# Kernel tuning notes

Hardware: AMD Instinct MI355X
Metric: run time of the kernel (lower is better)

Reference implementation:

```python
import jax, jax.numpy as jnp
import numpy as np

N, P, F, R, M = 20000, 320000, 128, 64, 32
F4 = F // 4            # n_atombasis // 4 == graph_n_messagebasis
L1 = 2                 # max_multipole_order + 1 (charges + dipoles)
N_BLOCKS = 2


def _w(key, fan_in, fan_out):
    return jax.random.normal(key, (fan_in, fan_out), dtype=jnp.float32) / np.sqrt(fan_in)


def setup_inputs() -> dict:
    key = jax.random.key(0)
    ks = jax.random.split(key, 24)
    inp = {
        'features': jax.random.normal(ks[0], (N, F), dtype=jnp.float32),
        'distances': jax.random.uniform(ks[1], (P,), dtype=jnp.float32),
        'vectors': jax.random.normal(ks[2], (P, 3), dtype=jnp.float32),
        'cutoffs': jax.random.uniform(ks[3], (P,), dtype=jnp.float32),
        'rbfs': jax.random.normal(ks[4], (P, R), dtype=jnp.float32),
        'idx_i': jnp.sort(jax.random.randint(ks[5], (P,), 0, N)),
        'idx_j': jax.random.randint(ks[6], (P,), 0, N),
    }
    d_inv = 6 * F4 + 2 * F   # (n_features_anisotropic+1)*(F//4) + 2*F = 448
    d_eq0 = F4 + 2 * F       # 288
    inp['Wrbf'] = _w(ks[7], R + 2 * F, F4)
    inp['Wemb'] = _w(ks[8], F, F)
    inp['eq0_W1'] = _w(ks[9], d_eq0, F)
    inp['eq0_b1'] = jnp.zeros((F,), jnp.float32)
    inp['eq0_W2'] = _w(ks[10], F, M * L1) * 0.01
    inp['eq1_W1'] = _w(ks[11], d_inv, F)
    inp['eq1_b1'] = jnp.zeros((F,), jnp.float32)
    inp['eq1_W2'] = _w(ks[12], F, M * L1) * 0.01
    inp['inv_W1'] = jnp.stack([_w(ks[13 + b], d_inv, F) for b in range(N_BLOCKS)])
    inp['inv_b1'] = jnp.zeros((N_BLOCKS, F), jnp.float32)
    inp['inv_W2'] = jnp.stack([_w(ks[15 + b], F, F) * 0.01 for b in range(N_BLOCKS)])
    inp['inv_b2'] = jnp.zeros((N_BLOCKS, F), jnp.float32)
    inp['upd_W1'] = jnp.stack([_w(ks[17 + b], 2 * F, F) for b in range(N_BLOCKS)])
    inp['upd_b1'] = jnp.zeros((N_BLOCKS, F), jnp.float32)
    inp['upd_W2'] = jnp.stack([_w(ks[19 + b], F, F) * 0.01 for b in range(N_BLOCKS)])
    inp['upd_b2'] = jnp.zeros((N_BLOCKS, F), jnp.float32)
    return inp


def reference(features, distances, vectors, cutoffs, rbfs, idx_i, idx_j,
              Wrbf, Wemb, eq0_W1, eq0_b1, eq0_W2, eq1_W1, eq1_b1, eq1_W2,
              inv_W1, inv_b1, inv_W2, inv_b2,
              upd_W1, upd_b1, upd_W2, upd_b2):
    silu = jax.nn.silu
    n_atoms = features.shape[0]
    # unit pair vectors (eps guards uniform distances near 0)
    u = vectors / (distances + 1e-3)[:, None]                 # [P,3]
    s = features                                              # [N,F] scalar features
    v = jnp.zeros((n_atoms, 3, M), dtype=features.dtype)      # [N,3,M] vector (dipole) features
    eq_params = [(eq0_W1, eq0_b1, eq0_W2), (eq1_W1, eq1_b1, eq1_W2)]
    for b in range(N_BLOCKS):
        si, sj = s[idx_i], s[idx_j]                           # gathers [P,F]
        e = jnp.concatenate([rbfs, si, sj], axis=-1) @ Wrbf   # pair embedding [P,F4]
        vi, vj = v[idx_i], v[idx_j]                           # [P,3,M]
        # anisotropic invariants of the equivariant features (5 of them, each [P,M])
        a_ui = jnp.einsum('pd,pdm->pm', u, vi)
        a_uj = jnp.einsum('pd,pdm->pm', u, vj)
        a_ij = jnp.sum(vi * vj, axis=1)
        a_ii = jnp.sum(vi * vi, axis=1)
        a_jj = jnp.sum(vj * vj, axis=1)
        x_inv = jnp.concatenate([e, a_ui, a_uj, a_ij, a_ii, a_jj, si, sj], axis=-1)  # [P,448]
        x_eq = jnp.concatenate([e, si, sj], axis=-1) if b == 0 else x_inv
        W1, b1, W2 = eq_params[b]
        g = silu(x_eq @ W1 + b1) @ W2                          # [P, M*2]
        g0, g1 = g[:, :M], g[:, M:]
        # equivariant message: radial direction term + propagated vector term
        dv = (g0[:, None, :] * u[:, :, None] + g1[:, None, :] * vj) * cutoffs[:, None, None]
        v = v + jax.ops.segment_sum(dv, idx_i, num_segments=n_atoms)
        # invariant message
        m = silu(silu(x_inv @ inv_W1[b] + inv_b1[b]) @ inv_W2[b] + inv_b2[b]) * cutoffs[:, None]
        s = s + jax.ops.segment_sum(m, idx_i, num_segments=n_atoms)
        # atom-wise update
        femb = s @ Wemb
        h = jnp.concatenate([s, femb], axis=-1)
        s = s + silu(silu(h @ upd_W1[b] + upd_b1[b]) @ upd_W2[b] + upd_b2[b])
    return s, v
```

## Files before the change

kernel.cpp:

```cpp
#include <hip/hip_runtime.h>
#include <math.h>

#define NA   20000
#define PE   320000
#define FDIM 128
#define ET   64
#define AT   32

typedef unsigned short ushort_t;
typedef __attribute__((ext_vector_type(8))) short bf16x8;
typedef __attribute__((ext_vector_type(4))) float f32x4;
#define MFMA16 __builtin_amdgcn_mfma_f32_16x16x32_bf16

#define XSTR     456
#define HSTR     136
#define XS_OFF   0
#define H1_OFF   58368
#define US_OFF   75776
#define IIS_OFF  76800
#define JJS_OFF  77064
#define SMEM_SZ  77320
#define ML_OFF   0
#define GL_OFF   33792

#define PK_W1EQ0   0
#define PK_W1EQ1   7168
#define PK_W1INV0  14336
#define PK_W1INV1  21504
#define PK_W2EQ0   28672
#define PK_W2EQ1   29696
#define PK_W2INV0  30720
#define PK_W2INV1  32768
#define PK_WRBF    34816
#define PK_WEMB    36096
#define PK_W1U0    38144
#define PK_W1U1    42240
#define PK_W2U0    46336
#define PK_W2U1    48384
#define PK_TOTAL   50432

__device__ __forceinline__ float silu_f(float z) {
    return z / (1.0f + __expf(-z));
}

__device__ __forceinline__ ushort_t f2bf(float x) {
    __bf16 h = (__bf16)x;
    union { __bf16 b; ushort_t u; } c; c.b = h; return c.u;
}

__device__ __forceinline__ unsigned int pack2bf(float x, float y) {
    return (unsigned int)f2bf(x) | ((unsigned int)f2bf(y) << 16);
}

__device__ __forceinline__ uint4 cvt8(float4 a, float4 b) {
    uint4 r;
    r.x = pack2bf(a.x, a.y); r.y = pack2bf(a.z, a.w);
    r.z = pack2bf(b.x, b.y); r.w = pack2bf(b.z, b.w);
    return r;
}

__global__ void pack_all(const float* __restrict__ eq0W1, const float* __restrict__ eq1W1,
                         const float* __restrict__ invW1, const float* __restrict__ eq0W2,
                         const float* __restrict__ eq1W2, const float* __restrict__ invW2,
                         const float* __restrict__ Wrbf,  const float* __restrict__ Wemb,
                         const float* __restrict__ updW1, const float* __restrict__ updW2,
                         ushort_t* __restrict__ out)
{
    const int tid = blockIdx.x * blockDim.x + threadIdx.x;
    if (tid >= PK_TOTAL) return;
    int base, KB, N, mode = 0;
    const float* src;
    if      (tid < PK_W1EQ1)  { base = PK_W1EQ0;  KB = 14; N = 128; src = eq0W1; mode = 1; }
    else if (tid < PK_W1INV0) { base = PK_W1EQ1;  KB = 14; N = 128; src = eq1W1; }
    else if (tid < PK_W1INV1) { base = PK_W1INV0; KB = 14; N = 128; src = invW1; }
    else if (tid < PK_W2EQ0)  { base = PK_W1INV1; KB = 14; N = 128; src = invW1 + 448 * 128; }
    else if (tid < PK_W2EQ1)  { base = PK_W2EQ0;  KB = 4;  N = 64;  src = eq0W2; }
    else if (tid < PK_W2INV0) { base = PK_W2EQ1;  KB = 4;  N = 64;  src = eq1W2; }
    else if (tid < PK_W2INV1) { base = PK_W2INV0; KB = 4;  N = 128; src = invW2; }
    else if (tid < PK_WRBF)   { base = PK_W2INV1; KB = 4;  N = 128; src = invW2 + 128 * 128; }
    else if (tid < PK_WEMB)   { base = PK_WRBF;   KB = 10; N = 32;  src = Wrbf; }
    else if (tid < PK_W1U0)   { base = PK_WEMB;   KB = 4;  N = 128; src = Wemb; }
    else if (tid < PK_W1U1)   { base = PK_W1U0;   KB = 8;  N = 128; src = updW1; }
    else if (tid < PK_W2U0)   { base = PK_W1U1;   KB = 8;  N = 128; src = updW1 + 256 * 128; }
    else if (tid < PK_W2U1)   { base = PK_W2U0;   KB = 4;  N = 128; src = updW2; }
    else                      { base = PK_W2U1;   KB = 4;  N = 128; src = updW2 + 128 * 128; }
    const int local = tid - base;
    const int lane  = local & 63;
    const int rest  = local >> 6;
    const int kb    = rest % KB;
    const int ct    = rest / KB;
    const int col   = ct * 16 + (lane & 15);
    const int k0    = kb * 32 + ((lane >> 4) * 8);
    ushort_t v[8];
    #pragma unroll
    for (int j = 0; j < 8; j++) {
        const int k = k0 + j;
        float x;
        if (mode == 1) x = (k < 32) ? src[k * N + col] : (k < 192 ? 0.f : src[(k - 160) * N + col]);
        else           x = src[(size_t)k * N + col];
        v[j] = f2bf(x);
    }
    *(uint4*)(out + (size_t)tid * 8) = *(uint4*)v;
}

__global__ __launch_bounds__(512, 4)
void edge_kernel(const float* __restrict__ rbfs,
                 const float* __restrict__ dists,
                 const float* __restrict__ vecs,
                 const float* __restrict__ cuts,
                 const int*   __restrict__ gidx_i,
                 const int*   __restrict__ gidx_j,
                 const ushort_t* __restrict__ s_bf,
                 const float* __restrict__ v_in,
                 const ushort_t* __restrict__ pWrbf,
                 const ushort_t* __restrict__ pW1eq,
                 const float* __restrict__ b1eq,
                 const ushort_t* __restrict__ pW2eq,
                 const ushort_t* __restrict__ pW1inv,
                 const float* __restrict__ b1inv,
                 const ushort_t* __restrict__ pW2inv,
                 const float* __restrict__ b2inv,
                 float* __restrict__ s_out,
                 float* __restrict__ v_out,
                 const int eqSkip)
{
    __shared__ __align__(16) char smem[SMEM_SZ];
    ushort_t* xs  = (ushort_t*)(smem + XS_OFF);
    ushort_t* h1  = (ushort_t*)(smem + H1_OFF);
    float*    us  = (float*)(smem + US_OFF);
    int*      iis = (int*)(smem + IIS_OFF);
    int*      jjs = (int*)(smem + JJS_OFF);
    float*    ml  = (float*)(smem + ML_OFF);
    float*    gl  = (float*)(smem + GL_OFF);

    const int t    = threadIdx.x;
    const int p0   = blockIdx.x * ET;
    const int lane = t & 63;
    const int wid  = t >> 6;
    const int colf = lane & 15;
    const int krow = (lane >> 4) * 8;

    {
        const int e = t >> 3, l = t & 7;
        const int p = p0 + e;
        const int i = gidx_i[p];
        const int j = gidx_j[p];
        const uint4* si4 = (const uint4*)(s_bf + (size_t)i * FDIM);
        const uint4* sj4 = (const uint4*)(s_bf + (size_t)j * FDIM);
        *(uint4*)&xs[e * XSTR + 192 + l * 16]     = si4[l * 2];
        *(uint4*)&xs[e * XSTR + 192 + l * 16 + 8] = si4[l * 2 + 1];
        *(uint4*)&xs[e * XSTR + 320 + l * 16]     = sj4[l * 2];
        *(uint4*)&xs[e * XSTR + 320 + l * 16 + 8] = sj4[l * 2 + 1];
        const float4* rb4 = (const float4*)(rbfs + (size_t)p * 64);
        float4 r0 = rb4[l * 2], r1 = rb4[l * 2 + 1];
        *(uint4*)&h1[e * HSTR + l * 8] = cvt8(r0, r1);
        if (t < ET) {
            const int pp = p0 + t;
            const float dinv = 1.0f / (dists[pp] + 0.001f);
            float4 uu;
            uu.x = vecs[pp * 3 + 0] * dinv;
            uu.y = vecs[pp * 3 + 1] * dinv;
            uu.z = vecs[pp * 3 + 2] * dinv;
            uu.w = cuts[pp];
            *(float4*)&us[t * 4] = uu;
            jjs[t] = gidx_j[pp];
        }
        if (t < ET + 1) {
            const int pp = p0 + t;
            iis[t] = (pp < PE) ? gidx_i[pp] : -1;
        }
    }
    __syncthreads();

    {
        const int e  = t >> 3;
        const int m0 = (t & 7) * 4;
        const int i = iis[e];
        const int j = jjs[e];
        float vi[3][4], vj[3][4];
        #pragma unroll
        for (int d = 0; d < 3; d++) {
            const float4 a = *(const float4*)(v_in + (size_t)i * 96 + d * 32 + m0);
            const float4 b = *(const float4*)(v_in + (size_t)j * 96 + d * 32 + m0);
            vi[d][0] = a.x; vi[d][1] = a.y; vi[d][2] = a.z; vi[d][3] = a.w;
            vj[d][0] = b.x; vj[d][1] = b.y; vj[d][2] = b.z; vj[d][3] = b.w;
        }
        const float ux = us[e * 4 + 0], uy = us[e * 4 + 1], uz = us[e * 4 + 2];
        float aui[4], auj[4], aij[4], aii[4], ajj[4];
        #pragma unroll
        for (int mm = 0; mm < 4; mm++) {
            aui[mm] = ux * vi[0][mm] + uy * vi[1][mm] + uz * vi[2][mm];
            auj[mm] = ux * vj[0][mm] + uy * vj[1][mm] + uz * vj[2][mm];
            aij[mm] = vi[0][mm] * vj[0][mm] + vi[1][mm] * vj[1][mm] + vi[2][mm] * vj[2][mm];
            aii[mm] = vi[0][mm] * vi[0][mm] + vi[1][mm] * vi[1][mm] + vi[2][mm] * vi[2][mm];
            ajj[mm] = vj[0][mm] * vj[0][mm] + vj[1][mm] * vj[1][mm] + vj[2][mm] * vj[2][mm];
        }
        uint2 w;
        w.x = pack2bf(aui[0], aui[1]); w.y = pack2bf(aui[2], aui[3]);
        *(uint2*)&xs[e * XSTR + 32 + m0] = w;
        w.x = pack2bf(auj[0], auj[1]); w.y = pack2bf(auj[2], auj[3]);
        *(uint2*)&xs[e * XSTR + 64 + m0] = w;
        w.x = pack2bf(aij[0], aij[1]); w.y = pack2bf(aij[2], aij[3]);
        *(uint2*)&xs[e * XSTR + 96 + m0] = w;
        w.x = pack2bf(aii[0], aii[1]); w.y = pack2bf(aii[2], aii[3]);
        *(uint2*)&xs[e * XSTR + 128 + m0] = w;
        w.x = pack2bf(ajj[0], ajj[1]); w.y = pack2bf(ajj[2], ajj[3]);
        *(uint2*)&xs[e * XSTR + 160 + m0] = w;
    }

    {
        const int rt = wid & 3;
        const int ct = wid >> 2;
        f32x4 eacc = {0.f, 0.f, 0.f, 0.f};
        #pragma unroll
        for (int kb = 0; kb < 10; kb++) {
            bf16x8 bf = *(const bf16x8*)(pWrbf + ((size_t)(ct * 10 + kb) * 64 + lane) * 8);
            bf16x8 af;
            if (kb < 2) af = *(const bf16x8*)&h1[(rt * 16 + colf) * HSTR + kb * 32 + krow];
            else        af = *(const bf16x8*)&xs[(rt * 16 + colf) * XSTR + 128 + kb * 32 + krow];
            eacc = MFMA16(af, bf, eacc, 0, 0, 0);
        }
        #pragma unroll
        for (int r = 0; r < 4; r++) {
            const int row = rt * 16 + (lane >> 4) * 4 + r;
            xs[row * XSTR + ct * 16 + colf] = f2bf(eacc[r]);
        }
    }
    __syncthreads();

    f32x4 ainv[4];
    {
        f32x4 aeq[4];
        const float bce = b1eq[wid * 16 + colf];
        const float bci = b1inv[wid * 16 + colf];
        #pragma unroll
        for (int rt = 0; rt < 4; rt++) {
            aeq[rt]  = (f32x4){bce, bce, bce, bce};
            ainv[rt] = (f32x4){bci, bci, bci, bci};
        }
        #pragma unroll
        for (int kb = 0; kb < 14; kb++) {
            bf16x8 af[4];
            #pragma unroll
            for (int rt = 0; rt < 4; rt++)
                af[rt] = *(const bf16x8*)&xs[(rt * 16 + colf) * XSTR + kb * 32 + krow];
            bf16x8 bi = *(const bf16x8*)(pW1inv + ((size_t)(wid * 14 + kb) * 64 + lane) * 8);
            #pragma unroll
            for (int rt = 0; rt < 4; rt++)
                ainv[rt] = MFMA16(af[rt], bi, ainv[rt], 0, 0, 0);
            if (!(eqSkip && kb >= 1 && kb < 6)) {
                bf16x8 be = *(const bf16x8*)(pW1eq + ((size_t)(wid * 14 + kb) * 64 + lane) * 8);
                #pragma unroll
                for (int rt = 0; rt < 4; rt++)
                    aeq[rt] = MFMA16(af[rt], be, aeq[rt], 0, 0, 0);
            }
        }
        #pragma unroll
        for (int rt = 0; rt < 4; rt++)
            #pragma unroll
            for (int r = 0; r < 4; r++) {
                const int row = rt * 16 + (lane >> 4) * 4 + r;
                h1[row * HSTR + wid * 16 + colf] = f2bf(silu_f(aeq[rt][r]));
            }
    }
    __syncthreads();

    f32x4 gacc[2];
    const int ct2 = wid & 3;
    const int rh  = wid >> 2;
    {
        gacc[0] = (f32x4){0.f, 0.f, 0.f, 0.f};
        gacc[1] = (f32x4){0.f, 0.f, 0.f, 0.f};
        #pragma unroll
        for (int kb = 0; kb < 4; kb++) {
            bf16x8 bf = *(const bf16x8*)(pW2eq + ((size_t)(ct2 * 4 + kb) * 64 + lane) * 8);
            #pragma unroll
            for (int q = 0; q < 2; q++) {
                bf16x8 af = *(const bf16x8*)&h1[((rh * 2 + q) * 16 + colf) * HSTR + kb * 32 + krow];
                gacc[q] = MFMA16(af, bf, gacc[q], 0, 0, 0);
            }
        }
    }
    __syncthreads();

    {
        #pragma unroll
        for (int rt = 0; rt < 4; rt++)
            #pragma unroll
            for (int r = 0; r < 4; r++) {
                const int row = rt * 16 + (lane >> 4) * 4 + r;
                h1[row * HSTR + wid * 16 + colf] = f2bf(silu_f(ainv[rt][r]));
            }
        #pragma unroll
        for (int q = 0; q < 2; q++)
            #pragma unroll
            for (int r = 0; r < 4; r++) {
                const int row = (rh * 2 + q) * 16 + (lane >> 4) * 4 + r;
                gl[row * 68 + ct2 * 16 + colf] = gacc[q][r];
            }
    }
    __syncthreads();

    {
        f32x4 macc[4];
        const float bc = b2inv[wid * 16 + colf];
        #pragma unroll
        for (int rt = 0; rt < 4; rt++) macc[rt] = (f32x4){bc, bc, bc, bc};
        #pragma unroll
        for (int kb = 0; kb < 4; kb++) {
            bf16x8 bf = *(const bf16x8*)(pW2inv + ((size_t)(wid * 4 + kb) * 64 + lane) * 8);
            #pragma unroll
            for (int rt = 0; rt < 4; rt++) {
                bf16x8 af = *(const bf16x8*)&h1[(rt * 16 + colf) * HSTR + kb * 32 + krow];
                macc[rt] = MFMA16(af, bf, macc[rt], 0, 0, 0);
            }
        }
        #pragma unroll
        for (int rt = 0; rt < 4; rt++)
            #pragma unroll
            for (int r = 0; r < 4; r++) {
                const int row = rt * 16 + (lane >> 4) * 4 + r;
                ml[row * 132 + wid * 16 + colf] = silu_f(macc[rt][r]) * us[row * 4 + 3];
            }
    }
    __syncthreads();

    {
        const int half = t >> 8;
        const int tl   = t & 255;
        if (tl < 224) {
            const int e0 = half * 32;
            if (tl < FDIM) {
                float acc = 0.f;
                for (int e = e0; e < e0 + 32; e++) {
                    acc += ml[e * 132 + tl];
                    if (e == e0 + 31 || iis[e + 1] != iis[e]) {
                        atomicAdd(&s_out[(size_t)iis[e] * FDIM + tl], acc);
                        acc = 0.f;
                    }
                }
            } else {
                const int col = tl - FDIM;
                const int d   = col >> 5;
                const int mm  = col & 31;
                float acc = 0.f;
                for (int e = e0; e < e0 + 32; e++) {
                    const float g0  = gl[e * 68 + mm];
                    const float g1  = gl[e * 68 + 32 + mm];
                    const float vjv = v_in[(size_t)jjs[e] * 96 + col];
                    acc = fmaf(us[e * 4 + 3], fmaf(g0, us[e * 4 + d], g1 * vjv), acc);
                    if (e == e0 + 31 || iis[e + 1] != iis[e]) {
                        atomicAdd(&v_out[(size_t)iis[e] * 96 + col], acc);
                        acc = 0.f;
                    }
                }
            }
        }
    }
}

__global__ __launch_bounds__(256, 4)
void node_kernel(const float* __restrict__ s_in,
                 const ushort_t* __restrict__ pWemb,
                 const ushort_t* __restrict__ pW1u,
                 const float* __restrict__ b1u,
                 const ushort_t* __restrict__ pW2u,
                 const float* __restrict__ b2u,
                 float* __restrict__ s_out,
                 ushort_t* __restrict__ sbf_out)
{
    __shared__ ushort_t ss[AT * HSTR];
    __shared__ ushort_t fe[AT * HSTR];
    __shared__ ushort_t t1[AT * HSTR];
    const int t    = threadIdx.x;
    const int a0   = blockIdx.x * AT;
    const int lane = t & 63;
    const int wid  = t >> 6;
    const int colf = lane & 15;
    const int krow = (lane >> 4) * 8;

    {
        const int a = t >> 3, l = t & 7;
        const float4* sr = (const float4*)(s_in + (size_t)(a0 + a) * FDIM);
        float4 q0 = sr[l * 4 + 0], q1 = sr[l * 4 + 1], q2 = sr[l * 4 + 2], q3 = sr[l * 4 + 3];
        *(uint4*)&ss[a * HSTR + l * 16]     = cvt8(q0, q1);
        *(uint4*)&ss[a * HSTR + l * 16 + 8] = cvt8(q2, q3);
    }
    __syncthreads();

    #pragma unroll
    for (int ci = 0; ci < 2; ci++) {
        const int ct = wid * 2 + ci;
        f32x4 acc[2];
        acc[0] = (f32x4){0.f, 0.f, 0.f, 0.f};
        acc[1] = (f32x4){0.f, 0.f, 0.f, 0.f};
        #pragma unroll
        for (int kb = 0; kb < 4; kb++) {
            bf16x8 bf = *(const bf16x8*)(pWemb + ((size_t)(ct * 4 + kb) * 64 + lane) * 8);
            #pragma unroll
            for (int rt = 0; rt < 2; rt++) {
                bf16x8 af = *(const bf16x8*)&ss[(rt * 16 + colf) * HSTR + kb * 32 + krow];
                acc[rt] = MFMA16(af, bf, acc[rt], 0, 0, 0);
            }
        }
        #pragma unroll
        for (int rt = 0; rt < 2; rt++)
            #pragma unroll
            for (int r = 0; r < 4; r++) {
                const int row = rt * 16 + (lane >> 4) * 4 + r;
                fe[row * HSTR + ct * 16 + colf] = f2bf(acc[rt][r]);
            }
    }
    __syncthreads();

    #pragma unroll
    for (int ci = 0; ci < 2; ci++) {
        const int ct = wid * 2 + ci;
        const float bc = b1u[ct * 16 + colf];
        f32x4 acc[2];
        acc[0] = (f32x4){bc, bc, bc, bc};
        acc[1] = (f32x4){bc, bc, bc, bc};
        #pragma unroll
        for (int kb = 0; kb < 8; kb++) {
            bf16x8 bf = *(const bf16x8*)(pW1u + ((size_t)(ct * 8 + kb) * 64 + lane) * 8);
            #pragma unroll
            for (int rt = 0; rt < 2; rt++) {
                bf16x8 af;
                if (kb < 4) af = *(const bf16x8*)&ss[(rt * 16 + colf) * HSTR + kb * 32 + krow];
                else        af = *(const bf16x8*)&fe[(rt * 16 + colf) * HSTR + (kb - 4) * 32 + krow];
                acc[rt] = MFMA16(af, bf, acc[rt], 0, 0, 0);
            }
        }
        #pragma unroll
        for (int rt = 0; rt < 2; rt++)
            #pragma unroll
            for (int r = 0; r < 4; r++) {
                const int row = rt * 16 + (lane >> 4) * 4 + r;
                t1[row * HSTR + ct * 16 + colf] = f2bf(silu_f(acc[rt][r]));
            }
    }
    __syncthreads();

    #pragma unroll
    for (int ci = 0; ci < 2; ci++) {
        const int ct = wid * 2 + ci;
        const float bc = b2u[ct * 16 + colf];
        f32x4 acc[2];
        acc[0] = (f32x4){bc, bc, bc, bc};
        acc[1] = (f32x4){bc, bc, bc, bc};
        #pragma unroll
        for (int kb = 0; kb < 4; kb++) {
            bf16x8 bf = *(const bf16x8*)(pW2u + ((size_t)(ct * 4 + kb) * 64 + lane) * 8);
            #pragma unroll
            for (int rt = 0; rt < 2; rt++) {
                bf16x8 af = *(const bf16x8*)&t1[(rt * 16 + colf) * HSTR + kb * 32 + krow];
                acc[rt] = MFMA16(af, bf, acc[rt], 0, 0, 0);
            }
        }
        #pragma unroll
        for (int rt = 0; rt < 2; rt++)
            #pragma unroll
            for (int r = 0; r < 4; r++) {
                const int row = rt * 16 + (lane >> 4) * 4 + r;
                const size_t off = (size_t)(a0 + row) * FDIM + ct * 16 + colf;
                const float o = s_in[off] + silu_f(acc[rt][r]);
                s_out[off] = o;
                sbf_out[off] = f2bf(o);
            }
    }
}

__global__ void copyf4(float4* __restrict__ dst, const float4* __restrict__ src, int n4) {
    int i = blockIdx.x * blockDim.x + threadIdx.x;
    const int stride = gridDim.x * blockDim.x;
    for (; i < n4; i += stride) dst[i] = src[i];
}

__global__ void zerof4(float4* __restrict__ dst, int n4) {
    int i = blockIdx.x * blockDim.x + threadIdx.x;
    const int stride = gridDim.x * blockDim.x;
    const float4 z = make_float4(0.f, 0.f, 0.f, 0.f);
    for (; i < n4; i += stride) dst[i] = z;
}

__global__ void cvt_bf(const float* __restrict__ in, ushort_t* __restrict__ out, int n8) {
    int i = blockIdx.x * blockDim.x + threadIdx.x;
    if (i < n8) {
        const float4* s = (const float4*)(in + (size_t)i * 8);
        *(uint4*)(out + (size_t)i * 8) = cvt8(s[0], s[1]);
    }
}

extern "C" void kernel_launch(void* const* d_in, const int* in_sizes, int n_in,
                              void* d_out, int out_size, void* d_ws, size_t ws_size,
                              hipStream_t stream) {
    (void)in_sizes; (void)n_in; (void)out_size; (void)ws_size;

    const float* features = (const float*)d_in[0];
    const float* dists    = (const float*)d_in[1];
    const float* vecs     = (const float*)d_in[2];
    const float* cuts     = (const float*)d_in[3];
    const float* rbfs     = (const float*)d_in[4];
    const int*   idx_i    = (const int*)d_in[5];
    const int*   idx_j    = (const int*)d_in[6];
    const float* Wrbf     = (const float*)d_in[7];
    const float* Wemb     = (const float*)d_in[8];
    const float* eq0_W1   = (const float*)d_in[9];
    const float* eq0_b1   = (const float*)d_in[10];
    const float* eq0_W2   = (const float*)d_in[11];
    const float* eq1_W1   = (const float*)d_in[12];
    const float* eq1_b1   = (const float*)d_in[13];
    const float* eq1_W2   = (const float*)d_in[14];
    const float* inv_W1   = (const float*)d_in[15];
    const float* inv_b1   = (const float*)d_in[16];
    const float* inv_W2   = (const float*)d_in[17];
    const float* inv_b2   = (const float*)d_in[18];
    const float* upd_W1   = (const float*)d_in[19];
    const float* upd_b1   = (const float*)d_in[20];
    const float* upd_W2   = (const float*)d_in[21];
    const float* upd_b2   = (const float*)d_in[22];

    float*    sA  = (float*)d_ws;
    float*    sB  = sA + (size_t)NA * FDIM;
    float*    vA  = sB + (size_t)NA * FDIM;
    float*    vB  = vA + (size_t)NA * 96;
    ushort_t* sbf = (ushort_t*)(vB + (size_t)NA * 96);
    ushort_t* pwb = sbf + (size_t)NA * FDIM;

    float* s_final = (float*)d_out;
    float* v_final = s_final + (size_t)NA * FDIM;

    const int SN4 = NA * FDIM / 4;
    const int VN4 = NA * 96 / 4;

    pack_all<<<(PK_TOTAL + 255) / 256, 256, 0, stream>>>(
        eq0_W1, eq1_W1, inv_W1, eq0_W2, eq1_W2, inv_W2, Wrbf, Wemb, upd_W1, upd_W2, pwb);
    cvt_bf<<<(NA * FDIM / 8 + 255) / 256, 256, 0, stream>>>(features, sbf, NA * FDIM / 8);
    copyf4<<<1024, 256, 0, stream>>>((float4*)sB, (const float4*)features, SN4);
    zerof4<<<1024, 256, 0, stream>>>((float4*)vA, VN4);
    zerof4<<<1024, 256, 0, stream>>>((float4*)vB, VN4);

    edge_kernel<<<PE / ET, 512, 0, stream>>>(
        rbfs, dists, vecs, cuts, idx_i, idx_j, sbf, vA,
        pwb + (size_t)PK_WRBF * 8,
        pwb + (size_t)PK_W1EQ0 * 8, eq0_b1, pwb + (size_t)PK_W2EQ0 * 8,
        pwb + (size_t)PK_W1INV0 * 8, inv_b1, pwb + (size_t)PK_W2INV0 * 8, inv_b2,
        sB, vB, 1);
    node_kernel<<<NA / AT, 256, 0, stream>>>(
        sB, pwb + (size_t)PK_WEMB * 8, pwb + (size_t)PK_W1U0 * 8, upd_b1,
        pwb + (size_t)PK_W2U0 * 8, upd_b2, sA, sbf);

    copyf4<<<1024, 256, 0, stream>>>((float4*)sB, (const float4*)sA, SN4);
    copyf4<<<1024, 256, 0, stream>>>((float4*)vA, (const float4*)vB, VN4);
    edge_kernel<<<PE / ET, 512, 0, stream>>>(
        rbfs, dists, vecs, cuts, idx_i, idx_j, sbf, vB,
        pwb + (size_t)PK_WRBF * 8,
        pwb + (size_t)PK_W1EQ1 * 8, eq1_b1, pwb + (size_t)PK_W2EQ1 * 8,
        pwb + (size_t)PK_W1INV1 * 8, inv_b1 + FDIM, pwb + (size_t)PK_W2INV1 * 8, inv_b2 + FDIM,
        sB, vA, 0);
    node_kernel<<<NA / AT, 256, 0, stream>>>(
        sB, pwb + (size_t)PK_WEMB * 8, pwb + (size_t)PK_W1U1 * 8, upd_b1 + FDIM,
        pwb + (size_t)PK_W2U1 * 8, upd_b2 + FDIM, s_final, sbf);

    copyf4<<<1024, 256, 0, stream>>>((float4*)v_final, (const float4*)vA, VN4);
}
```

Measured before the change: 653.9 us.

## Fold RBF projection into first-layer weights and restructure edge kernel scatter

Folds the Wrbf projection into the first-layer eq and inv weights when they are packed. The edge kernel now feeds raw RBFs (K=480) straight into the fused GEMM, which removes the separate rbf MFMA stage and one barrier. The anisotropic features are computed in the load phase and skipped in block 0. The change also remaps block indices for locality, splits the s/v scatter across more threads, and raises node kernel occupancy. It drops the intermediate s/v copies by writing in place into sA and v_final. The folded weights are rounded to bf16 after the product, which changes numerics slightly.

```diff
diff --git a/kernel.cpp b/kernel.cpp
--- a/kernel.cpp
+++ b/kernel.cpp
@@ -12,32 +12,31 @@
 typedef __attribute__((ext_vector_type(4))) float f32x4;
 #define MFMA16 __builtin_amdgcn_mfma_f32_16x16x32_bf16
 
-#define XSTR     456
-#define HSTR     136
+#define XSTR     482
+#define HSTR     132
 #define XS_OFF   0
-#define H1_OFF   58368
-#define US_OFF   75776
-#define IIS_OFF  76800
-#define JJS_OFF  77064
-#define SMEM_SZ  77320
-#define ML_OFF   0
-#define GL_OFF   33792
+#define H1_OFF   61696
+#define US_OFF   78592
+#define IIS_OFF  79616
+#define JJS_OFF  79876
+#define SMEM_SZ  80136
+#define GL_OFF   0
+#define ML_OFF   17408
 
 #define PK_W1EQ0   0
-#define PK_W1EQ1   7168
-#define PK_W1INV0  14336
-#define PK_W1INV1  21504
-#define PK_W2EQ0   28672
-#define PK_W2EQ1   29696
-#define PK_W2INV0  30720
-#define PK_W2INV1  32768
-#define PK_WRBF    34816
-#define PK_WEMB    36096
-#define PK_W1U0    38144
-#define PK_W1U1    42240
-#define PK_W2U0    46336
-#define PK_W2U1    48384
-#define PK_TOTAL   50432
+#define PK_W1EQ1   7680
+#define PK_W1INV0  15360
+#define PK_W1INV1  23040
+#define PK_W2EQ0   30720
+#define PK_W2EQ1   31744
+#define PK_W2INV0  32768
+#define PK_W2INV1  34816
+#define PK_WEMB    36864
+#define PK_W1U0    38912
+#define PK_W1U1    43008
+#define PK_W2U0    47104
+#define PK_W2U1    49152
+#define PK_TOTAL   51200
 
 __device__ __forceinline__ float silu_f(float z) {
     return z / (1.0f + __expf(-z));
@@ -68,17 +67,16 @@
 {
     const int tid = blockIdx.x * blockDim.x + threadIdx.x;
     if (tid >= PK_TOTAL) return;
-    int base, KB, N, mode = 0;
+    int base, KB, N, fused = 0, mode = 0;
     const float* src;
-    if      (tid < PK_W1EQ1)  { base = PK_W1EQ0;  KB = 14; N = 128; src = eq0W1; mode = 1; }
-    else if (tid < PK_W1INV0) { base = PK_W1EQ1;  KB = 14; N = 128; src = eq1W1; }
-    else if (tid < PK_W1INV1) { base = PK_W1INV0; KB = 14; N = 128; src = invW1; }
-    else if (tid < PK_W2EQ0)  { base = PK_W1INV1; KB = 14; N = 128; src = invW1 + 448 * 128; }
+    if      (tid < PK_W1EQ1)  { base = PK_W1EQ0;  KB = 15; N = 128; src = eq0W1; fused = 1; mode = 1; }
+    else if (tid < PK_W1INV0) { base = PK_W1EQ1;  KB = 15; N = 128; src = eq1W1; fused = 1; }
+    else if (tid < PK_W1INV1) { base = PK_W1INV0; KB = 15; N = 128; src = invW1; fused = 1; }
+    else if (tid < PK_W2EQ0)  { base = PK_W1INV1; KB = 15; N = 128; src = invW1 + 448 * 128; fused = 1; }
     else if (tid < PK_W2EQ1)  { base = PK_W2EQ0;  KB = 4;  N = 64;  src = eq0W2; }
     else if (tid < PK_W2INV0) { base = PK_W2EQ1;  KB = 4;  N = 64;  src = eq1W2; }
     else if (tid < PK_W2INV1) { base = PK_W2INV0; KB = 4;  N = 128; src = invW2; }
-    else if (tid < PK_WRBF)   { base = PK_W2INV1; KB = 4;  N = 128; src = invW2 + 128 * 128; }
-    else if (tid < PK_WEMB)   { base = PK_WRBF;   KB = 10; N = 32;  src = Wrbf; }
+    else if (tid < PK_WEMB)   { base = PK_W2INV1; KB = 4;  N = 128; src = invW2 + 128 * 128; }
     else if (tid < PK_W1U0)   { base = PK_WEMB;   KB = 4;  N = 128; src = Wemb; }
     else if (tid < PK_W1U1)   { base = PK_W1U0;   KB = 8;  N = 128; src = updW1; }
     else if (tid < PK_W2U0)   { base = PK_W1U1;   KB = 8;  N = 128; src = updW1 + 256 * 128; }
@@ -96,8 +94,21 @@
     for (int j = 0; j < 8; j++) {
         const int k = k0 + j;
         float x;
-        if (mode == 1) x = (k < 32) ? src[k * N + col] : (k < 192 ? 0.f : src[(k - 160) * N + col]);
-        else           x = src[(size_t)k * N + col];
+        if (!fused) {
+            x = src[(size_t)k * N + col];
+        } else {
+            x = 0.f;
+            const int di = (mode == 0) ? (k >= 64 ? k - 32 : -1)
+                                       : (k >= 224 ? k - 192 : -1);
+            if (di >= 0) x = src[(size_t)di * 128 + col];
+            const int dr = (k < 64) ? k : (k >= 224 ? k - 160 : -1);
+            if (dr >= 0) {
+                float s = 0.f;
+                for (int q = 0; q < 32; q++)
+                    s += Wrbf[dr * 32 + q] * src[(size_t)q * 128 + col];
+                x += s;
+            }
+        }
         v[j] = f2bf(x);
     }
     *(uint4*)(out + (size_t)tid * 8) = *(uint4*)v;
@@ -112,7 +123,6 @@
                  const int*   __restrict__ gidx_j,
                  const ushort_t* __restrict__ s_bf,
                  const float* __restrict__ v_in,
-                 const ushort_t* __restrict__ pWrbf,
                  const ushort_t* __restrict__ pW1eq,
                  const float* __restrict__ b1eq,
                  const ushort_t* __restrict__ pW2eq,
@@ -130,11 +140,12 @@
     float*    us  = (float*)(smem + US_OFF);
     int*      iis = (int*)(smem + IIS_OFF);
     int*      jjs = (int*)(smem + JJS_OFF);
+    float*    gl  = (float*)(smem + GL_OFF);
     float*    ml  = (float*)(smem + ML_OFF);
-    float*    gl  = (float*)(smem + GL_OFF);
 
     const int t    = threadIdx.x;
-    const int p0   = blockIdx.x * ET;
+    const int bid  = blockIdx.x;
+    const int p0   = ((bid & 7) * 625 + (bid >> 3)) * ET;
     const int lane = t & 63;
     const int wid  = t >> 6;
     const int colf = lane & 15;
@@ -147,13 +158,13 @@
         const int j = gidx_j[p];
         const uint4* si4 = (const uint4*)(s_bf + (size_t)i * FDIM);
         const uint4* sj4 = (const uint4*)(s_bf + (size_t)j * FDIM);
-        *(uint4*)&xs[e * XSTR + 192 + l * 16]     = si4[l * 2];
-        *(uint4*)&xs[e * XSTR + 192 + l * 16 + 8] = si4[l * 2 + 1];
-        *(uint4*)&xs[e * XSTR + 320 + l * 16]     = sj4[l * 2];
-        *(uint4*)&xs[e * XSTR + 320 + l * 16 + 8] = sj4[l * 2 + 1];
+        *(uint4*)&xs[e * XSTR + 224 + l * 16]     = si4[l * 2];
+        *(uint4*)&xs[e * XSTR + 224 + l * 16 + 8] = si4[l * 2 + 1];
+        *(uint4*)&xs[e * XSTR + 352 + l * 16]     = sj4[l * 2];
+        *(uint4*)&xs[e * XSTR + 352 + l * 16 + 8] = sj4[l * 2 + 1];
         const float4* rb4 = (const float4*)(rbfs + (size_t)p * 64);
         float4 r0 = rb4[l * 2], r1 = rb4[l * 2 + 1];
-        *(uint4*)&h1[e * HSTR + l * 8] = cvt8(r0, r1);
+        *(uint4*)&xs[e * XSTR + l * 8] = cvt8(r0, r1);
         if (t < ET) {
             const int pp = p0 + t;
             const float dinv = 1.0f / (dists[pp] + 0.001f);
@@ -169,61 +180,40 @@
             const int pp = p0 + t;
             iis[t] = (pp < PE) ? gidx_i[pp] : -1;
         }
-    }
-    __syncthreads();
-
-    {
-        const int e  = t >> 3;
-        const int m0 = (t & 7) * 4;
-        const int i = iis[e];
-        const int j = jjs[e];
-        float vi[3][4], vj[3][4];
-        #pragma unroll
-        for (int d = 0; d < 3; d++) {
-            const float4 a = *(const float4*)(v_in + (size_t)i * 96 + d * 32 + m0);
-            const float4 b = *(const float4*)(v_in + (size_t)j * 96 + d * 32 + m0);
-            vi[d][0] = a.x; vi[d][1] = a.y; vi[d][2] = a.z; vi[d][3] = a.w;
-            vj[d][0] = b.x; vj[d][1] = b.y; vj[d][2] = b.z; vj[d][3] = b.w;
-        }
-        const float ux = us[e * 4 + 0], uy = us[e * 4 + 1], uz = us[e * 4 + 2];
-        float aui[4], auj[4], aij[4], aii[4], ajj[4];
-        #pragma unroll
-        for (int mm = 0; mm < 4; mm++) {
-            aui[mm] = ux * vi[0][mm] + uy * vi[1][mm] + uz * vi[2][mm];
-            auj[mm] = ux * vj[0][mm] + uy * vj[1][mm] + uz * vj[2][mm];
-            aij[mm] = vi[0][mm] * vj[0][mm] + vi[1][mm] * vj[1][mm] + vi[2][mm] * vj[2][mm];
-            aii[mm] = vi[0][mm] * vi[0][mm] + vi[1][mm] * vi[1][mm] + vi[2][mm] * vi[2][mm];
-            ajj[mm] = vj[0][mm] * vj[0][mm] + vj[1][mm] * vj[1][mm] + vj[2][mm] * vj[2][mm];
-        }
-        uint2 w;
-        w.x = pack2bf(aui[0], aui[1]); w.y = pack2bf(aui[2], aui[3]);
-        *(uint2*)&xs[e * XSTR + 32 + m0] = w;
-        w.x = pack2bf(auj[0], auj[1]); w.y = pack2bf(auj[2], auj[3]);
-        *(uint2*)&xs[e * XSTR + 64 + m0] = w;
-        w.x = pack2bf(aij[0], aij[1]); w.y = pack2bf(aij[2], aij[3]);
-        *(uint2*)&xs[e * XSTR + 96 + m0] = w;
-        w.x = pack2bf(aii[0], aii[1]); w.y = pack2bf(aii[2], aii[3]);
-        *(uint2*)&xs[e * XSTR + 128 + m0] = w;
-        w.x = pack2bf(ajj[0], ajj[1]); w.y = pack2bf(ajj[2], ajj[3]);
-        *(uint2*)&xs[e * XSTR + 160 + m0] = w;
-    }
-
-    {
-        const int rt = wid & 3;
-        const int ct = wid >> 2;
-        f32x4 eacc = {0.f, 0.f, 0.f, 0.f};
-        #pragma unroll
-        for (int kb = 0; kb < 10; kb++) {
-            bf16x8 bf = *(const bf16x8*)(pWrbf + ((size_t)(ct * 10 + kb) * 64 + lane) * 8);
-            bf16x8 af;
-            if (kb < 2) af = *(const bf16x8*)&h1[(rt * 16 + colf) * HSTR + kb * 32 + krow];
-            else        af = *(const bf16x8*)&xs[(rt * 16 + colf) * XSTR + 128 + kb * 32 + krow];
-            eacc = MFMA16(af, bf, eacc, 0, 0, 0);
-        }
-        #pragma unroll
-        for (int r = 0; r < 4; r++) {
-            const int row = rt * 16 + (lane >> 4) * 4 + r;
-            xs[row * XSTR + ct * 16 + colf] = f2bf(eacc[r]);
+        if (!eqSkip) {
+            const int m0 = (t & 7) * 4;
+            const float dinv = 1.0f / (dists[p] + 0.001f);
+            const float ux = vecs[p * 3 + 0] * dinv;
+            const float uy = vecs[p * 3 + 1] * dinv;
+            const float uz = vecs[p * 3 + 2] * dinv;
+            float vi[3][4], vj[3][4];
+            #pragma unroll
+            for (int d = 0; d < 3; d++) {
+                const float4 a = *(const float4*)(v_in + (size_t)i * 96 + d * 32 + m0);
+                const float4 b = *(const float4*)(v_in + (size_t)j * 96 + d * 32 + m0);
+                vi[d][0] = a.x; vi[d][1] = a.y; vi[d][2] = a.z; vi[d][3] = a.w;
+                vj[d][0] = b.x; vj[d][1] = b.y; vj[d][2] = b.z; vj[d][3] = b.w;
+            }
+            float aui[4], auj[4], aij[4], aii[4], ajj[4];
+            #pragma unroll
+            for (int mm = 0; mm < 4; mm++) {
+                aui[mm] = ux * vi[0][mm] + uy * vi[1][mm] + uz * vi[2][mm];
+                auj[mm] = ux * vj[0][mm] + uy * vj[1][mm] + uz * vj[2][mm];
+                aij[mm] = vi[0][mm] * vj[0][mm] + vi[1][mm] * vj[1][mm] + vi[2][mm] * vj[2][mm];
+                aii[mm] = vi[0][mm] * vi[0][mm] + vi[1][mm] * vi[1][mm] + vi[2][mm] * vi[2][mm];
+                ajj[mm] = vj[0][mm] * vj[0][mm] + vj[1][mm] * vj[1][mm] + vj[2][mm] * vj[2][mm];
+            }
+            uint2 w;
+            w.x = pack2bf(aui[0], aui[1]); w.y = pack2bf(aui[2], aui[3]);
+            *(uint2*)&xs[e * XSTR + 64 + m0] = w;
+            w.x = pack2bf(auj[0], auj[1]); w.y = pack2bf(auj[2], auj[3]);
+            *(uint2*)&xs[e * XSTR + 96 + m0] = w;
+            w.x = pack2bf(aij[0], aij[1]); w.y = pack2bf(aij[2], aij[3]);
+            *(uint2*)&xs[e * XSTR + 128 + m0] = w;
+            w.x = pack2bf(aii[0], aii[1]); w.y = pack2bf(aii[2], aii[3]);
+            *(uint2*)&xs[e * XSTR + 160 + m0] = w;
+            w.x = pack2bf(ajj[0], ajj[1]); w.y = pack2bf(ajj[2], ajj[3]);
+            *(uint2*)&xs[e * XSTR + 192 + m0] = w;
         }
     }
     __syncthreads();
@@ -239,21 +229,20 @@
             ainv[rt] = (f32x4){bci, bci, bci, bci};
         }
         #pragma unroll
-        for (int kb = 0; kb < 14; kb++) {
+        for (int kb = 0; kb < 15; kb++) {
+            if (eqSkip && kb >= 2 && kb < 7) continue;
             bf16x8 af[4];
             #pragma unroll
             for (int rt = 0; rt < 4; rt++)
                 af[rt] = *(const bf16x8*)&xs[(rt * 16 + colf) * XSTR + kb * 32 + krow];
-            bf16x8 bi = *(const bf16x8*)(pW1inv + ((size_t)(wid * 14 + kb) * 64 + lane) * 8);
+            bf16x8 bi = *(const bf16x8*)(pW1inv + ((size_t)(wid * 15 + kb) * 64 + lane) * 8);
             #pragma unroll
             for (int rt = 0; rt < 4; rt++)
                 ainv[rt] = MFMA16(af[rt], bi, ainv[rt], 0, 0, 0);
-            if (!(eqSkip && kb >= 1 && kb < 6)) {
-                bf16x8 be = *(const bf16x8*)(pW1eq + ((size_t)(wid * 14 + kb) * 64 + lane) * 8);
-                #pragma unroll
-                for (int rt = 0; rt < 4; rt++)
-                    aeq[rt] = MFMA16(af[rt], be, aeq[rt], 0, 0, 0);
-            }
+            bf16x8 be = *(const bf16x8*)(pW1eq + ((size_t)(wid * 15 + kb) * 64 + lane) * 8);
+            #pragma unroll
+            for (int rt = 0; rt < 4; rt++)
+                aeq[rt] = MFMA16(af[rt], be, aeq[rt], 0, 0, 0);
         }
         #pragma unroll
         for (int rt = 0; rt < 4; rt++)
@@ -265,10 +254,10 @@
     }
     __syncthreads();
 
-    f32x4 gacc[2];
-    const int ct2 = wid & 3;
-    const int rh  = wid >> 2;
-    {
+    {
+        const int ct2 = wid & 3;
+        const int rh  = wid >> 2;
+        f32x4 gacc[2];
         gacc[0] = (f32x4){0.f, 0.f, 0.f, 0.f};
         gacc[1] = (f32x4){0.f, 0.f, 0.f, 0.f};
         #pragma unroll
@@ -280,6 +269,13 @@
                 gacc[q] = MFMA16(af, bf, gacc[q], 0, 0, 0);
             }
         }
+        #pragma unroll
+        for (int q = 0; q < 2; q++)
+            #pragma unroll
+            for (int r = 0; r < 4; r++) {
+                const int row = (rh * 2 + q) * 16 + (lane >> 4) * 4 + r;
+                gl[row * 68 + ct2 * 16 + colf] = gacc[q][r];
+            }
     }
     __syncthreads();
 
@@ -290,13 +286,6 @@
             for (int r = 0; r < 4; r++) {
                 const int row = rt * 16 + (lane >> 4) * 4 + r;
                 h1[row * HSTR + wid * 16 + colf] = f2bf(silu_f(ainv[rt][r]));
-            }
-        #pragma unroll
-        for (int q = 0; q < 2; q++)
-            #pragma unroll
-            for (int r = 0; r < 4; r++) {
-                const int row = (rh * 2 + q) * 16 + (lane >> 4) * 4 + r;
-                gl[row * 68 + ct2 * 16 + colf] = gacc[q][r];
             }
     }
     __syncthreads();
@@ -326,40 +315,41 @@
     __syncthreads();
 
     {
-        const int half = t >> 8;
-        const int tl   = t & 255;
-        if (tl < 224) {
-            const int e0 = half * 32;
-            if (tl < FDIM) {
-                float acc = 0.f;
-                for (int e = e0; e < e0 + 32; e++) {
-                    acc += ml[e * 132 + tl];
-                    if (e == e0 + 31 || iis[e + 1] != iis[e]) {
-                        atomicAdd(&s_out[(size_t)iis[e] * FDIM + tl], acc);
-                        acc = 0.f;
-                    }
-                }
-            } else {
-                const int col = tl - FDIM;
-                const int d   = col >> 5;
-                const int mm  = col & 31;
-                float acc = 0.f;
-                for (int e = e0; e < e0 + 32; e++) {
-                    const float g0  = gl[e * 68 + mm];
-                    const float g1  = gl[e * 68 + 32 + mm];
-                    const float vjv = v_in[(size_t)jjs[e] * 96 + col];
-                    acc = fmaf(us[e * 4 + 3], fmaf(g0, us[e * 4 + d], g1 * vjv), acc);
-                    if (e == e0 + 31 || iis[e + 1] != iis[e]) {
-                        atomicAdd(&v_out[(size_t)iis[e] * 96 + col], acc);
-                        acc = 0.f;
-                    }
-                }
-            }
-        }
-    }
-}
-
-__global__ __launch_bounds__(256, 4)
+        const int qq = t >> 7;
+        const int c  = t & 127;
+        const int e0 = qq * 16;
+        float acc = 0.f;
+        #pragma unroll
+        for (int e = e0; e < e0 + 16; e++) {
+            acc += ml[e * 132 + c];
+            if (e == e0 + 15 || iis[e + 1] != iis[e]) {
+                atomicAdd(&s_out[(size_t)iis[e] * FDIM + c], acc);
+                acc = 0.f;
+            }
+        }
+    }
+    if (t < 384) {
+        const int qq  = t / 96;
+        const int c   = t - qq * 96;
+        const int d   = c >> 5;
+        const int mm  = c & 31;
+        const int e0  = qq * 16;
+        float acc = 0.f;
+        #pragma unroll
+        for (int e = e0; e < e0 + 16; e++) {
+            const float g0  = gl[e * 68 + mm];
+            const float g1  = gl[e * 68 + 32 + mm];
+            const float vjv = v_in[(size_t)jjs[e] * 96 + c];
+            acc = fmaf(us[e * 4 + 3], fmaf(g0, us[e * 4 + d], g1 * vjv), acc);
+            if (e == e0 + 15 || iis[e + 1] != iis[e]) {
+                atomicAdd(&v_out[(size_t)iis[e] * 96 + c], acc);
+                acc = 0.f;
+            }
+        }
+    }
+}
+
+__global__ __launch_bounds__(256, 6)
 void node_kernel(const float* __restrict__ s_in,
                  const ushort_t* __restrict__ pWemb,
                  const ushort_t* __restrict__ pW1u,
@@ -542,7 +532,6 @@
 
     edge_kernel<<<PE / ET, 512, 0, stream>>>(
         rbfs, dists, vecs, cuts, idx_i, idx_j, sbf, vA,
-        pwb + (size_t)PK_WRBF * 8,
         pwb + (size_t)PK_W1EQ0 * 8, eq0_b1, pwb + (size_t)PK_W2EQ0 * 8,
         pwb + (size_t)PK_W1INV0 * 8, inv_b1, pwb + (size_t)PK_W2INV0 * 8, inv_b2,
         sB, vB, 1);
@@ -550,17 +539,13 @@
         sB, pwb + (size_t)PK_WEMB * 8, pwb + (size_t)PK_W1U0 * 8, upd_b1,
         pwb + (size_t)PK_W2U0 * 8, upd_b2, sA, sbf);
 
-    copyf4<<<1024, 256, 0, stream>>>((float4*)sB, (const float4*)sA, SN4);
-    copyf4<<<1024, 256, 0, stream>>>((float4*)vA, (const float4*)vB, VN4);
+    copyf4<<<1024, 256, 0, stream>>>((float4*)v_final, (const float4*)vB, VN4);
     edge_kernel<<<PE / ET, 512, 0, stream>>>(
         rbfs, dists, vecs, cuts, idx_i, idx_j, sbf, vB,
-        pwb + (size_t)PK_WRBF * 8,
         pwb + (size_t)PK_W1EQ1 * 8, eq1_b1, pwb + (size_t)PK_W2EQ1 * 8,
         pwb + (size_t)PK_W1INV1 * 8, inv_b1 + FDIM, pwb + (size_t)PK_W2INV1 * 8, inv_b2 + FDIM,
-        sB, vA, 0);
+        sA, v_final, 0);
     node_kernel<<<NA / AT, 256, 0, stream>>>(
-        sB, pwb + (size_t)PK_WEMB * 8, pwb + (size_t)PK_W1U1 * 8, upd_b1 + FDIM,
+        sA, pwb + (size_t)PK_WEMB * 8, pwb + (size_t)PK_W1U1 * 8, upd_b1 + FDIM,
         pwb + (size_t)PK_W2U1 * 8, upd_b2 + FDIM, s_final, sbf);
-
-    copyf4<<<1024, 256, 0, stream>>>((float4*)v_final, (const float4*)vA, VN4);
-}
+}
```

Result: slower. 1.060 ms (+62.1%).
